# Kernel tuning notes

Hardware: AMD Instinct MI355X
Metric: run time of the kernel (lower is better)

Reference implementation:

```python
import jax, jax.numpy as jnp
import numpy as np

NUM_STEPS = 10
NUM_NODES = 100000
NUM_EDGES = 6400000


def setup_inputs() -> dict:
    key = jax.random.key(0)
    k1, k2, k3 = jax.random.split(key, 3)
    x = jax.random.uniform(k1, (NUM_NODES, 1), dtype=jnp.float32)
    edge_index = jax.random.randint(k2, (2, NUM_EDGES), 0, NUM_NODES, dtype=jnp.int64)
    edge_probs = jax.random.uniform(k3, (NUM_EDGES,), dtype=jnp.float32)
    # learned parameters (match torch init)
    time_decay = jnp.linspace(0.0, 1.0, NUM_STEPS, dtype=jnp.float32)
    node_bias = jnp.float32(0.0)
    edge_weight = jnp.ones((NUM_STEPS,), dtype=jnp.float32)
    return {
        "x": x,
        "edge_index": edge_index,
        "edge_probs": edge_probs,
        "time_decay": time_decay,
        "node_bias": node_bias,
        "edge_weight": edge_weight,
    }


def reference(x, edge_index, edge_probs, time_decay, node_bias, edge_weight):
    src, dst = edge_index[0], edge_index[1]
    num_nodes = x.shape[0]
    # per-step scalar scale: edge_weight[i] * exp(-time_decay[i]^2)
    step_scale = edge_weight * jnp.exp(-(time_decay ** 2))  # (num_steps,)

    def step(carry, scale):
        cur, surv = carry
        # gather node state to edges, scale, scatter-add back to nodes
        messages = cur[src] * (edge_probs[:, None] * scale)  # (num_edges, 1)
        cur = jax.ops.segment_sum(messages, dst, num_segments=num_nodes)
        cur = cur + node_bias
        surv = surv * (1.0 - cur)
        return (cur, surv), None

    (_, survival_prob), _ = jax.lax.scan(step, (x, 1.0 - x), step_scale)
    final_infection = 1.0 - survival_prob
    return jnp.clip(final_infection, 0.0, 1.0)
```

## Files before the change

### kernel.cpp

```cpp
#include <hip/hip_runtime.h>
#include <math.h>


#define MAXBINS     64
#define BIN_SHIFT   11
#define BIN_SIZE    2048
#define STAGE_CAP   64
#define BUCKET_GRID 1024
#define BUCKET_TPB  256
#define BUCKET_K    8
#define STEP_TPB    256

__global__ void k_detect(const unsigned long long* ei, int* flag) {
    if (blockIdx.x == 0 && threadIdx.x == 0) {
        int is64 = 1;
        for (int k = 0; k < 64; ++k)
            if ((ei[k] >> 32) != 0ULL) { is64 = 0; break; }
        *flag = is64;
    }
}

__global__ void k_scales(const float* __restrict__ time_decay,
                         const float* __restrict__ edge_weight,
                         float* __restrict__ step_scale, int num_steps,
                         unsigned int* __restrict__ gcur) {
    int i = threadIdx.x;
    if (i < num_steps) {
        float td = time_decay[i];
        step_scale[i] = edge_weight[i] * expf(-td * td);
    }
    if (i < MAXBINS) gcur[i] = 0u;
}

__global__ void k_init(const float* __restrict__ x, float* __restrict__ cur0,
                       float* __restrict__ surv, int n) {
    int i = blockIdx.x * blockDim.x + threadIdx.x;
    if (i < n) {
        float v = x[i];
        cur0[i] = v;
        surv[i] = 1.0f - v;
    }
}

__global__ void k_bucket(const void* __restrict__ ei_raw, const int* __restrict__ flag,
                         const float* __restrict__ probs, unsigned int* __restrict__ gcur,
                         float2* __restrict__ sorted, unsigned int capr,
                         int E, int nbins) {
    __shared__ float2 buf[MAXBINS][STAGE_CAP];
    __shared__ unsigned int cnt[MAXBINS];
    __shared__ unsigned int gbase[MAXBINS];
    const int t = threadIdx.x;
    const int wid = t >> 6, lane = t & 63;
    const int nwaves = BUCKET_TPB / 64;
    const int is64 = *flag;
    const int chunk = (E + gridDim.x - 1) / gridDim.x;
    const int beg = blockIdx.x * chunk;
    const int end = min(E, beg + chunk);
    for (int i = t; i < nbins; i += BUCKET_TPB) cnt[i] = 0u;
    __syncthreads();
    const int ROUND = BUCKET_TPB * BUCKET_K;
    for (int rbeg = beg; rbeg < end; rbeg += ROUND) {
        for (int k = 0; k < BUCKET_K; ++k) {
            int e = rbeg + k * BUCKET_TPB + t;
            if (e < end) {
                int src, dst;
                if (is64) {
                    const long long* s = (const long long*)ei_raw;
                    src = (int)s[e]; dst = (int)s[e + E];
                } else {
                    const int* s = (const int*)ei_raw;
                    src = s[e]; dst = s[e + E];
                }
                float pr = probs[e];
                int bin = dst >> BIN_SHIFT;
                unsigned int payload = (unsigned int)src |
                                       ((unsigned int)(dst & (BIN_SIZE - 1)) << 17);
                unsigned int pos = atomicAdd(&cnt[bin], 1u);
                if (pos < STAGE_CAP) {
                    buf[bin][pos] = make_float2(__uint_as_float(payload), pr);
                } else {
                    unsigned int gp = atomicAdd(&gcur[bin], 1u);
                    if (gp < capr)
                        sorted[(size_t)bin * capr + gp] =
                            make_float2(__uint_as_float(payload), pr);
                }
            }
        }
        __syncthreads();
        if (t < nbins) {
            unsigned int c = min(cnt[t], (unsigned int)STAGE_CAP);
            if (c > 0u) gbase[t] = atomicAdd(&gcur[t], c);
        }
        __syncthreads();
        for (int b = wid; b < nbins; b += nwaves) {
            unsigned int c = min(cnt[b], (unsigned int)STAGE_CAP);
            if ((unsigned int)lane < c) {
                unsigned int gp = gbase[b] + (unsigned int)lane;
                if (gp < capr)
                    sorted[(size_t)b * capr + gp] = buf[b][lane];
            }
        }
        __syncthreads();
        for (int i = t; i < nbins; i += BUCKET_TPB) cnt[i] = 0u;
        __syncthreads();
    }
}

__global__ void __launch_bounds__(STEP_TPB)
k_step(const float2* __restrict__ sorted, const unsigned int* __restrict__ gcur,
       const float* __restrict__ cur_in, float* __restrict__ part,
       unsigned int capr, int pstride, int nbins, int splits) {
    __shared__ float acc[BIN_SIZE];
    const int bin = blockIdx.x / splits;
    const int sp  = blockIdx.x - bin * splits;
    const int t = threadIdx.x;
    for (int i = t; i < BIN_SIZE; i += STEP_TPB) acc[i] = 0.0f;
    __syncthreads();
    unsigned int cntv = min(gcur[bin], capr);
    unsigned int sub = ((cntv + (unsigned int)splits - 1) / (unsigned int)splits + 3u) & ~3u;
    unsigned int s0 = min(cntv, (unsigned int)sp * sub);
    unsigned int s1 = min(cntv, s0 + sub);
    const float2* base = sorted + (size_t)bin * capr;
    for (unsigned int j = s0 + (unsigned int)t * 4u; j < s1; j += STEP_TPB * 4u) {
        if (j + 4u <= s1) {
            float4 a = *reinterpret_cast<const float4*>(base + j);
            float4 b = *reinterpret_cast<const float4*>(base + j + 2);
            unsigned int k0 = __float_as_uint(a.x), k1 = __float_as_uint(a.z);
            unsigned int k2 = __float_as_uint(b.x), k3 = __float_as_uint(b.z);
            float m0 = cur_in[k0 & 0x1FFFFu] * a.y;
            float m1 = cur_in[k1 & 0x1FFFFu] * a.w;
            float m2 = cur_in[k2 & 0x1FFFFu] * b.y;
            float m3 = cur_in[k3 & 0x1FFFFu] * b.w;
            atomicAdd(&acc[k0 >> 17], m0);
            atomicAdd(&acc[k1 >> 17], m1);
            atomicAdd(&acc[k2 >> 17], m2);
            atomicAdd(&acc[k3 >> 17], m3);
        } else {
            for (unsigned int q = j; q < s1; ++q) {
                float2 kp = base[q];
                unsigned int k = __float_as_uint(kp.x);
                atomicAdd(&acc[k >> 17], cur_in[k & 0x1FFFFu] * kp.y);
            }
        }
    }
    __syncthreads();
    float* dst = part + (size_t)sp * pstride + (size_t)bin * BIN_SIZE;
    for (int i = t; i < BIN_SIZE; i += STEP_TPB)
        dst[i] = acc[i];
}

__global__ void k_reduce(const float* __restrict__ part, int pstride, int splits,
                         float* __restrict__ cur_out, float* __restrict__ surv,
                         const float* __restrict__ step_scale, const float* __restrict__ bias_p,
                         float* __restrict__ out, int step, int n, int last) {
    int i = blockIdx.x * blockDim.x + threadIdx.x;
    if (i >= n) return;
    float c = 0.0f;
    for (int s = 0; s < splits; ++s) c += part[(size_t)s * pstride + i];
    c = c * step_scale[step] + bias_p[0];
    if (!last) cur_out[i] = c;
    float sv = surv[i] * (1.0f - c);
    surv[i] = sv;
    if (last) out[i] = fminf(fmaxf(1.0f - sv, 0.0f), 1.0f);
}

__global__ void k_init0(const float* __restrict__ x, float* __restrict__ cur,
                        float* __restrict__ surv, float* __restrict__ acc, int n) {
    int i = blockIdx.x * blockDim.x + threadIdx.x;
    if (i < n) {
        float v = x[i];
        cur[i] = v; surv[i] = 1.0f - v; acc[i] = 0.0f;
    }
}

__global__ void k_edge_raw(const void* __restrict__ ei_raw, const int* __restrict__ flag,
                           const float* __restrict__ probs, const float* __restrict__ cur,
                           float* __restrict__ acc, const float* __restrict__ step_scale,
                           int step, int num_edges) {
    const float scale = step_scale[step];
    const int is64 = *flag;
    const int stride = gridDim.x * blockDim.x;
    for (int e = blockIdx.x * blockDim.x + threadIdx.x; e < num_edges; e += stride) {
        int src, dst;
        if (is64) {
            const long long* s = (const long long*)ei_raw;
            src = (int)s[e]; dst = (int)s[e + num_edges];
        } else {
            const int* s = (const int*)ei_raw;
            src = s[e]; dst = s[e + num_edges];
        }
        atomicAdd(&acc[dst], cur[src] * (probs[e] * scale));
    }
}

__global__ void k_node(float* __restrict__ cur, float* __restrict__ acc,
                       float* __restrict__ surv, const float* __restrict__ bias_p,
                       float* __restrict__ out, int n, int write_out) {
    int i = blockIdx.x * blockDim.x + threadIdx.x;
    if (i < n) {
        float c = acc[i] + bias_p[0];
        acc[i] = 0.0f;
        cur[i] = c;
        float s = surv[i] * (1.0f - c);
        surv[i] = s;
        if (write_out) out[i] = fminf(fmaxf(1.0f - s, 0.0f), 1.0f);
    }
}

static inline size_t al256(size_t x) { return (x + 255) & ~(size_t)255; }

extern "C" void kernel_launch(void* const* d_in, const int* in_sizes, int n_in,
                              void* d_out, int out_size, void* d_ws, size_t ws_size,
                              hipStream_t stream) {
    const float* x           = (const float*)d_in[0];
    const void*  ei          = d_in[1];
    const float* probs       = (const float*)d_in[2];
    const float* time_decay  = (const float*)d_in[3];
    const float* node_bias   = (const float*)d_in[4];
    const float* edge_weight = (const float*)d_in[5];
    float* outf = (float*)d_out;

    const int n = in_sizes[0];
    const int E = in_sizes[2];
    const int S = in_sizes[3];

    char* ws = (char*)d_ws;
    int*          flag       = (int*)ws;
    float*        step_scale = (float*)(ws + 64);
    unsigned int* gcur       = (unsigned int*)(ws + 256);

    const int nbins   = (n + BIN_SIZE - 1) >> BIN_SHIFT;
    const int pstride = nbins * BIN_SIZE;

    const double   meand  = (double)E / (nbins > 0 ? nbins : 1);
    const double   sigma  = sqrt(meand > 1.0 ? meand : 1.0);
    unsigned int   want   = (unsigned int)(meand + 16.0 * sigma + 64.0);
    unsigned int   least  = (unsigned int)(meand + 6.0 * sigma + 64.0);
    want  = (want  + 63u) & ~63u;
    least = (least + 63u) & ~63u;

    const size_t nbA      = al256((size_t)n * 4);
    const size_t off_buf  = 512;
    const size_t off_surv = off_buf + nbA;
    const size_t off_part = al256(off_surv + nbA);

    int splits = 0;
    unsigned int capr = 0;
    size_t off_sort = 0;
    const int cand[5] = {40, 32, 24, 16, 8};
    for (int ci = 0; ci < 5; ++ci) {
        int sp = cand[ci];
        size_t part_b = (size_t)sp * pstride * 4;
        size_t osort  = al256(off_part + part_b);
        if (ws_size <= osort) continue;
        size_t availb = ws_size - osort;
        unsigned int acap = (unsigned int)((availb / ((size_t)nbins * 8)) & ~(size_t)63);
        if (acap >= least) {
            splits  = sp;
            capr    = acap < want ? acap : want;
            off_sort = osort;
            break;
        }
    }

    const int nthreads  = 256;
    const int node_grid = (n + nthreads - 1) / nthreads;

    const bool ok = (n <= (1 << 17)) && (nbins >= 1) && (nbins <= MAXBINS) &&
                    (E > 0) && (splits > 0);

    k_detect<<<1, 64, 0, stream>>>((const unsigned long long*)ei, flag);
    k_scales<<<1, 64, 0, stream>>>(time_decay, edge_weight, step_scale, S, gcur);

    if (!ok) {
        float* cur  = (float*)(ws + off_buf);
        float* surv = (float*)(ws + off_surv);
        float* acc  = (float*)(ws + off_surv + nbA);
        k_init0<<<node_grid, nthreads, 0, stream>>>(x, cur, surv, acc, n);
        for (int s = 0; s < S; ++s) {
            k_edge_raw<<<2048, nthreads, 0, stream>>>(ei, flag, probs, cur, acc,
                                                      step_scale, s, E);
            k_node<<<node_grid, nthreads, 0, stream>>>(cur, acc, surv, node_bias,
                                                       outf, n, s == S - 1 ? 1 : 0);
        }
        return;
    }

    float*  bufA   = (float*)(ws + off_buf);
    float*  surv   = (float*)(ws + off_surv);
    float*  part   = (float*)(ws + off_part);
    float2* sorted = (float2*)(ws + off_sort);

    float* b0 = (S % 2 == 0) ? outf : bufA;
    float* b1 = (S % 2 == 0) ? bufA : outf;

    k_init<<<node_grid, nthreads, 0, stream>>>(x, b0, surv, n);

    k_bucket<<<BUCKET_GRID, BUCKET_TPB, 0, stream>>>(ei, flag, probs, gcur, sorted,
                                                     capr, E, nbins);

    const int step_grid = nbins * splits;
    for (int s = 0; s < S; ++s) {
        float* ci = (s % 2 == 0) ? b0 : b1;
        float* co = (s % 2 == 0) ? b1 : b0;
        k_step<<<step_grid, STEP_TPB, 0, stream>>>(sorted, gcur, ci, part,
                                                   capr, pstride, nbins, splits);
        k_reduce<<<node_grid, nthreads, 0, stream>>>(part, pstride, splits, co, surv,
                                                     step_scale, node_bias, outf,
                                                     s, n, s == S - 1 ? 1 : 0);
    }
}
```

Before: 695.6 us.

## Fuse all propagation steps into one cooperative persistent kernel with grid syncs

Replaces the per-step pair of step and reduce launches with a single cooperative kernel that loops over all steps, using grid-wide syncs between the scatter phase and the node-update phase. To keep the grid co-resident, the split count is lowered (16/8/4, capped at 2048 blocks), and a second ping-pong buffer replaces the trick of writing into the output array. The bucket kernel's shared staging buffer is also repacked as padded floats to reduce LDS bank conflicts. This removes launch overhead and inter-kernel gaps, but adds two grid barriers per step and gives fewer blocks per bin, so there is less parallelism in the edge phase.

```diff
diff --git a/kernel.cpp b/kernel.cpp
--- a/kernel.cpp
+++ b/kernel.cpp
@@ -1,5 +1,8 @@
 #include <hip/hip_runtime.h>
+#include <hip/hip_cooperative_groups.h>
 #include <math.h>
+
+namespace cg = cooperative_groups;
 
 
 #define MAXBINS     64
@@ -46,7 +49,7 @@
                          const float* __restrict__ probs, unsigned int* __restrict__ gcur,
                          float2* __restrict__ sorted, unsigned int capr,
                          int E, int nbins) {
-    __shared__ float2 buf[MAXBINS][STAGE_CAP];
+    __shared__ float buf[MAXBINS][2 * STAGE_CAP + 1];
     __shared__ unsigned int cnt[MAXBINS];
     __shared__ unsigned int gbase[MAXBINS];
     const int t = threadIdx.x;
@@ -77,7 +80,8 @@
                                        ((unsigned int)(dst & (BIN_SIZE - 1)) << 17);
                 unsigned int pos = atomicAdd(&cnt[bin], 1u);
                 if (pos < STAGE_CAP) {
-                    buf[bin][pos] = make_float2(__uint_as_float(payload), pr);
+                    buf[bin][2 * pos]     = __uint_as_float(payload);
+                    buf[bin][2 * pos + 1] = pr;
                 } else {
                     unsigned int gp = atomicAdd(&gcur[bin], 1u);
                     if (gp < capr)
@@ -97,12 +101,78 @@
             if ((unsigned int)lane < c) {
                 unsigned int gp = gbase[b] + (unsigned int)lane;
                 if (gp < capr)
-                    sorted[(size_t)b * capr + gp] = buf[b][lane];
+                    sorted[(size_t)b * capr + gp] =
+                        make_float2(buf[b][2 * lane], buf[b][2 * lane + 1]);
             }
         }
         __syncthreads();
         for (int i = t; i < nbins; i += BUCKET_TPB) cnt[i] = 0u;
         __syncthreads();
+    }
+}
+
+__global__ void __launch_bounds__(STEP_TPB)
+k_steps(const float2* __restrict__ sorted, const unsigned int* __restrict__ gcur,
+        float* __restrict__ bufA, float* __restrict__ bufB,
+        float* __restrict__ surv, float* __restrict__ part,
+        const float* __restrict__ step_scale, const float* __restrict__ bias_p,
+        float* __restrict__ out,
+        unsigned int capr, int pstride, int splits, int n, int S) {
+    cg::grid_group grid = cg::this_grid();
+    __shared__ float acc[BIN_SIZE];
+    const int bid = blockIdx.x, t = threadIdx.x;
+    const int bin = bid / splits;
+    const int sp  = bid - bin * splits;
+    const unsigned int cntv = min(gcur[bin], capr);
+    unsigned int sub = ((cntv + (unsigned int)splits - 1) / (unsigned int)splits + 3u) & ~3u;
+    const unsigned int s0 = min(cntv, (unsigned int)sp * sub);
+    const unsigned int s1 = min(cntv, s0 + sub);
+    const float2* base = sorted + (size_t)bin * capr;
+    float* dstp = part + (size_t)sp * pstride + (size_t)bin * BIN_SIZE;
+    const int gsz = (int)gridDim.x * STEP_TPB;
+    for (int s = 0; s < S; ++s) {
+        const float* cur_in = (s & 1) ? bufB : bufA;
+        float*       cur_out = (s & 1) ? bufA : bufB;
+        for (int i = t; i < BIN_SIZE; i += STEP_TPB) acc[i] = 0.0f;
+        __syncthreads();
+        for (unsigned int j = s0 + (unsigned int)t * 4u; j < s1; j += STEP_TPB * 4u) {
+            if (j + 4u <= s1) {
+                float4 a = *reinterpret_cast<const float4*>(base + j);
+                float4 b = *reinterpret_cast<const float4*>(base + j + 2);
+                unsigned int k0 = __float_as_uint(a.x), k1 = __float_as_uint(a.z);
+                unsigned int k2 = __float_as_uint(b.x), k3 = __float_as_uint(b.z);
+                float m0 = cur_in[k0 & 0x1FFFFu] * a.y;
+                float m1 = cur_in[k1 & 0x1FFFFu] * a.w;
+                float m2 = cur_in[k2 & 0x1FFFFu] * b.y;
+                float m3 = cur_in[k3 & 0x1FFFFu] * b.w;
+                atomicAdd(&acc[k0 >> 17], m0);
+                atomicAdd(&acc[k1 >> 17], m1);
+                atomicAdd(&acc[k2 >> 17], m2);
+                atomicAdd(&acc[k3 >> 17], m3);
+            } else {
+                for (unsigned int q = j; q < s1; ++q) {
+                    float2 kp = base[q];
+                    unsigned int k = __float_as_uint(kp.x);
+                    atomicAdd(&acc[k >> 17], cur_in[k & 0x1FFFFu] * kp.y);
+                }
+            }
+        }
+        __syncthreads();
+        for (int i = t; i < BIN_SIZE; i += STEP_TPB) dstp[i] = acc[i];
+        grid.sync();
+        const float scale = step_scale[s];
+        const float bias  = bias_p[0];
+        const int last = (s == S - 1);
+        for (int i = bid * STEP_TPB + t; i < n; i += gsz) {
+            float c = 0.0f;
+            for (int r = 0; r < splits; ++r) c += part[(size_t)r * pstride + i];
+            c = c * scale + bias;
+            cur_out[i] = c;
+            float sv = surv[i] * (1.0f - c);
+            surv[i] = sv;
+            if (last) out[i] = fminf(fmaxf(1.0f - sv, 0.0f), 1.0f);
+        }
+        grid.sync();
     }
 }
 
@@ -127,14 +197,10 @@
             float4 b = *reinterpret_cast<const float4*>(base + j + 2);
             unsigned int k0 = __float_as_uint(a.x), k1 = __float_as_uint(a.z);
             unsigned int k2 = __float_as_uint(b.x), k3 = __float_as_uint(b.z);
-            float m0 = cur_in[k0 & 0x1FFFFu] * a.y;
-            float m1 = cur_in[k1 & 0x1FFFFu] * a.w;
-            float m2 = cur_in[k2 & 0x1FFFFu] * b.y;
-            float m3 = cur_in[k3 & 0x1FFFFu] * b.w;
-            atomicAdd(&acc[k0 >> 17], m0);
-            atomicAdd(&acc[k1 >> 17], m1);
-            atomicAdd(&acc[k2 >> 17], m2);
-            atomicAdd(&acc[k3 >> 17], m3);
+            atomicAdd(&acc[k0 >> 17], cur_in[k0 & 0x1FFFFu] * a.y);
+            atomicAdd(&acc[k1 >> 17], cur_in[k1 & 0x1FFFFu] * a.w);
+            atomicAdd(&acc[k2 >> 17], cur_in[k2 & 0x1FFFFu] * b.y);
+            atomicAdd(&acc[k3 >> 17], cur_in[k3 & 0x1FFFFu] * b.w);
         } else {
             for (unsigned int q = j; q < s1; ++q) {
                 float2 kp = base[q];
@@ -158,7 +224,7 @@
     float c = 0.0f;
     for (int s = 0; s < splits; ++s) c += part[(size_t)s * pstride + i];
     c = c * step_scale[step] + bias_p[0];
-    if (!last) cur_out[i] = c;
+    cur_out[i] = c;
     float sv = surv[i] * (1.0f - c);
     surv[i] = sv;
     if (last) out[i] = fminf(fmaxf(1.0f - sv, 0.0f), 1.0f);
@@ -240,16 +306,18 @@
     least = (least + 63u) & ~63u;
 
     const size_t nbA      = al256((size_t)n * 4);
-    const size_t off_buf  = 512;
-    const size_t off_surv = off_buf + nbA;
+    const size_t off_bufA = 512;
+    const size_t off_bufB = off_bufA + nbA;
+    const size_t off_surv = off_bufB + nbA;
     const size_t off_part = al256(off_surv + nbA);
 
     int splits = 0;
     unsigned int capr = 0;
     size_t off_sort = 0;
-    const int cand[5] = {40, 32, 24, 16, 8};
-    for (int ci = 0; ci < 5; ++ci) {
+    const int cand[3] = {16, 8, 4};
+    for (int ci = 0; ci < 3; ++ci) {
         int sp = cand[ci];
+        if ((long long)nbins * sp > 2048) continue;
         size_t part_b = (size_t)sp * pstride * 4;
         size_t osort  = al256(off_part + part_b);
         if (ws_size <= osort) continue;
@@ -273,9 +341,9 @@
     k_scales<<<1, 64, 0, stream>>>(time_decay, edge_weight, step_scale, S, gcur);
 
     if (!ok) {
-        float* cur  = (float*)(ws + off_buf);
+        float* cur  = (float*)(ws + off_bufA);
         float* surv = (float*)(ws + off_surv);
-        float* acc  = (float*)(ws + off_surv + nbA);
+        float* acc  = (float*)(ws + off_bufB);
         k_init0<<<node_grid, nthreads, 0, stream>>>(x, cur, surv, acc, n);
         for (int s = 0; s < S; ++s) {
             k_edge_raw<<<2048, nthreads, 0, stream>>>(ei, flag, probs, cur, acc,
@@ -286,23 +354,40 @@
         return;
     }
 
-    float*  bufA   = (float*)(ws + off_buf);
+    float*  bufA   = (float*)(ws + off_bufA);
+    float*  bufB   = (float*)(ws + off_bufB);
     float*  surv   = (float*)(ws + off_surv);
     float*  part   = (float*)(ws + off_part);
     float2* sorted = (float2*)(ws + off_sort);
 
-    float* b0 = (S % 2 == 0) ? outf : bufA;
-    float* b1 = (S % 2 == 0) ? bufA : outf;
-
-    k_init<<<node_grid, nthreads, 0, stream>>>(x, b0, surv, n);
+    k_init<<<node_grid, nthreads, 0, stream>>>(x, bufA, surv, n);
 
     k_bucket<<<BUCKET_GRID, BUCKET_TPB, 0, stream>>>(ei, flag, probs, gcur, sorted,
                                                      capr, E, nbins);
 
     const int step_grid = nbins * splits;
+
+    {
+        const float2* a_sorted = sorted;
+        const unsigned int* a_gcur = gcur;
+        float* a_bufA = bufA; float* a_bufB = bufB;
+        float* a_surv = surv; float* a_part = part;
+        const float* a_ss = step_scale; const float* a_bias = node_bias;
+        float* a_out = outf;
+        unsigned int a_capr = capr;
+        int a_pstride = pstride, a_splits = splits, a_n = n, a_S = S;
+        void* args[] = {&a_sorted, &a_gcur, &a_bufA, &a_bufB, &a_surv, &a_part,
+                        &a_ss, &a_bias, &a_out, &a_capr, &a_pstride, &a_splits,
+                        &a_n, &a_S};
+        hipError_t cerr = hipLaunchCooperativeKernel((const void*)k_steps,
+                                                     dim3(step_grid), dim3(STEP_TPB),
+                                                     args, 0, stream);
+        if (cerr == hipSuccess) return;
+    }
+
     for (int s = 0; s < S; ++s) {
-        float* ci = (s % 2 == 0) ? b0 : b1;
-        float* co = (s % 2 == 0) ? b1 : b0;
+        float* ci = (s & 1) ? bufB : bufA;
+        float* co = (s & 1) ? bufA : bufB;
         k_step<<<step_grid, STEP_TPB, 0, stream>>>(sorted, gcur, ci, part,
                                                    capr, pstride, nbins, splits);
         k_reduce<<<node_grid, nthreads, 0, stream>>>(part, pstride, splits, co, surv,
```

Result: slower. 2.765 ms (+297.5%).
